# Kernel tuning notes

Hardware: AMD Instinct MI355X
Metric: run time of the kernel (lower is better)

Reference implementation:

```python
import jax, jax.numpy as jnp
import numpy as np

INPUTS, L1, L2, L3 = 40960, 256, 32, 32
B, K = 16384, 32  # batch, fixed active features per side


def setup_inputs() -> dict:
    key = jax.random.key(0)
    ks = jax.random.split(key, 12)
    wf = jax.random.randint(ks[0], (B * K,), 0, INPUTS, dtype=jnp.int64)
    bf = jax.random.randint(ks[1], (B * K,), 0, INPUTS, dtype=jnp.int64)
    offs = jnp.arange(B, dtype=jnp.int64) * K
    stm = jax.random.uniform(ks[2], (B,), dtype=jnp.float32)
    table = jax.random.normal(ks[3], (INPUTS, L1), dtype=jnp.float32) * 0.01
    ft_bias = jnp.zeros((L1,), dtype=jnp.float32)
    # xavier_uniform bounds: sqrt(6/(fan_in+fan_out))
    def xavier(k, shape):
        bound = np.sqrt(6.0 / (shape[0] + shape[1]))
        return jax.random.uniform(k, shape, jnp.float32, -bound, bound)
    W1 = xavier(ks[4], (L2, 2 * L1)); b1 = jnp.zeros((L2,), jnp.float32)
    W2 = xavier(ks[5], (L3, L2));     b2 = jnp.zeros((L3,), jnp.float32)
    Wo = xavier(ks[6], (1, L3));      bo = jnp.zeros((1,), jnp.float32)
    return {"white_features": wf, "white_offsets": offs, "black_features": bf,
            "black_offsets": offs, "stm": stm, "table": table, "ft_bias": ft_bias,
            "W1": W1, "b1": b1, "W2": W2, "b2": b2, "Wo": Wo, "bo": bo}


def _crelu(x):
    return jnp.clip(x, 0.0, 1.0)


def reference(white_features, white_offsets, black_features, black_offsets, stm,
              table, ft_bias, W1, b1, W2, b2, Wo, bo):
    nb = white_offsets.shape[0]
    # Uniform-bag EmbeddingBag(mode='sum'): gather rows and sum within each bag.
    w_acc = table[white_features.reshape(nb, -1)].sum(axis=1) + ft_bias  # [B, L1]
    b_acc = table[black_features.reshape(nb, -1)].sum(axis=1) + ft_bias  # [B, L1]
    wtm = jnp.concatenate([w_acc, b_acc], axis=1)  # [B, 2*L1]
    btm = jnp.concatenate([b_acc, w_acc], axis=1)
    s = stm.reshape(-1, 1)
    x = _crelu(s * wtm + (1.0 - s) * btm)
    x = _crelu(x @ W1.T + b1)
    x = _crelu(x @ W2.T + b2)
    return (x @ Wo.T + bo).squeeze(1)  # [B]
```

## Files before the change

### kernel.cpp

```cpp
#include <hip/hip_runtime.h>

#define KFEAT 32
#define NB 8
#define XPITCH 544
#define APITCH 272

__device__ __forceinline__ float clip01(float v) {
    return fminf(fmaxf(v, 0.0f), 1.0f);
}

__global__ __launch_bounds__(256) void quantize_table_i8(
    const float* __restrict__ src, uint* __restrict__ qt,
    float* __restrict__ scales, int nrows)
{
    const int row = blockIdx.x * 4 + (threadIdx.x >> 6);
    const int l   = threadIdx.x & 63;
    if (row >= nrows) return;

    const float4 v = reinterpret_cast<const float4*>(src)[(size_t)row * 64 + l];
    float m = fmaxf(fmaxf(fabsf(v.x), fabsf(v.y)), fmaxf(fabsf(v.z), fabsf(v.w)));
    m = fmaxf(m, __shfl_xor(m, 1));
    m = fmaxf(m, __shfl_xor(m, 2));
    m = fmaxf(m, __shfl_xor(m, 4));
    m = fmaxf(m, __shfl_xor(m, 8));
    m = fmaxf(m, __shfl_xor(m, 16));
    m = fmaxf(m, __shfl_xor(m, 32));

    const float inv = (m > 0.0f) ? 127.0f / m : 0.0f;
    const int b0 = ((int)rintf(v.x * inv)) & 0xFF;
    const int b1 = ((int)rintf(v.y * inv)) & 0xFF;
    const int b2 = ((int)rintf(v.z * inv)) & 0xFF;
    const int b3 = ((int)rintf(v.w * inv)) & 0xFF;
    qt[(size_t)row * 64 + l] = (uint)b0 | ((uint)b1 << 8) | ((uint)b2 << 16) | ((uint)b3 << 24);
    if (l == 0) scales[row] = m * (1.0f / 127.0f);
}

__global__ __launch_bounds__(256, 8) void nnue_i8_kernel(
    const int* __restrict__ wf, const int* __restrict__ bf,
    const float* __restrict__ stm, const uint* __restrict__ qt,
    const float* __restrict__ scales,
    const float* __restrict__ ft_bias,
    const float* __restrict__ W1, const float* __restrict__ b1,
    const float* __restrict__ W2, const float* __restrict__ b2,
    const float* __restrict__ Wo, const float* __restrict__ bo,
    float* __restrict__ out)
{
    __shared__ float lds[NB * XPITCH];
    __shared__ float y1s[NB][32];

    const int t   = threadIdx.x;
    const int l   = t & 63;
    const int w   = t >> 6;
    const int sub = l & 31;
    const int b0  = blockIdx.x * NB;

    {
        const int side = w & 1;
        const int eb   = w >> 1;
        const int* fp  = side ? bf : wf;

        #pragma unroll
        for (int g = 0; g < 4; ++g) {
            const int bag  = g * 4 + w;
            const int iv   = fp[(size_t)(b0 + 2 * g + eb) * KFEAT + sub];
            float a0 = 0.f, a1 = 0.f, a2 = 0.f, a3 = 0.f;
            #pragma unroll
            for (int k = 0; k < KFEAT; ++k) {
                const int row  = __builtin_amdgcn_readlane(iv, k);
                const int  q   = (int)qt[(size_t)row * 64 + l];
                const float sc = scales[row];
                a0 = fmaf((float)((q << 24) >> 24), sc, a0);
                a1 = fmaf((float)((q << 16) >> 24), sc, a1);
                a2 = fmaf((float)((q <<  8) >> 24), sc, a2);
                a3 = fmaf((float)( q        >> 24), sc, a3);
            }
            *reinterpret_cast<float4*>(&lds[bag * APITCH + l * 4]) =
                make_float4(a0, a1, a2, a3);
        }
    }
    __syncthreads();

    {
        const int e = t >> 5, r = t & 31;
        const float s  = stm[b0 + e];
        const float os = 1.0f - s;
        const float4 wa0 = *reinterpret_cast<const float4*>(&lds[(2 * e + 0) * APITCH + 4 * r]);
        const float4 ba0 = *reinterpret_cast<const float4*>(&lds[(2 * e + 1) * APITCH + 4 * r]);
        const float4 wa1 = *reinterpret_cast<const float4*>(&lds[(2 * e + 0) * APITCH + 4 * (r + 32)]);
        const float4 ba1 = *reinterpret_cast<const float4*>(&lds[(2 * e + 1) * APITCH + 4 * (r + 32)]);
        const float4 fb0 = reinterpret_cast<const float4*>(ft_bias)[r];
        const float4 fb1 = reinterpret_cast<const float4*>(ft_bias)[r + 32];
        __syncthreads();

        #define MIXW(wa, ba, fb, i, hf)                                              \
        {                                                                            \
            float4 xv;                                                               \
            if (hf == 0) {                                                           \
                xv.x = clip01(fmaf(s, (wa).x, fmaf(os, (ba).x, (fb).x)));            \
                xv.y = clip01(fmaf(s, (wa).y, fmaf(os, (ba).y, (fb).y)));            \
                xv.z = clip01(fmaf(s, (wa).z, fmaf(os, (ba).z, (fb).z)));            \
                xv.w = clip01(fmaf(s, (wa).w, fmaf(os, (ba).w, (fb).w)));            \
            } else {                                                                 \
                xv.x = clip01(fmaf(s, (ba).x, fmaf(os, (wa).x, (fb).x)));            \
                xv.y = clip01(fmaf(s, (ba).y, fmaf(os, (wa).y, (fb).y)));            \
                xv.z = clip01(fmaf(s, (ba).z, fmaf(os, (wa).z, (fb).z)));            \
                xv.w = clip01(fmaf(s, (ba).w, fmaf(os, (wa).w, (fb).w)));            \
            }                                                                        \
            const int d = (hf) * 256 + 4 * (i);                                      \
            *reinterpret_cast<float4*>(&lds[e * XPITCH + (d >> 6) * 68 + (d & 63)]) = xv; \
        }
        MIXW(wa0, ba0, fb0, r,      0)
        MIXW(wa1, ba1, fb1, r + 32, 0)
        MIXW(wa0, ba0, fb0, r,      1)
        MIXW(wa1, ba1, fb1, r + 32, 1)
        #undef MIXW
    }
    __syncthreads();

    {
        const int j = t >> 3;
        const int c = t & 7;
        const float* w1p = W1 + j * 512 + c * 64;
        float acc[NB] = {0.f, 0.f, 0.f, 0.f, 0.f, 0.f, 0.f, 0.f};
        #pragma unroll
        for (int blk = 0; blk < 4; ++blk) {
            const float4 wv0 = reinterpret_cast<const float4*>(w1p + blk * 16)[0];
            const float4 wv1 = reinterpret_cast<const float4*>(w1p + blk * 16)[1];
            const float4 wv2 = reinterpret_cast<const float4*>(w1p + blk * 16)[2];
            const float4 wv3 = reinterpret_cast<const float4*>(w1p + blk * 16)[3];
            #pragma unroll
            for (int e = 0; e < NB; ++e) {
                const float* xp = &lds[e * XPITCH + c * 68 + blk * 16];
                const float4 x0 = *reinterpret_cast<const float4*>(xp + 0);
                const float4 x1 = *reinterpret_cast<const float4*>(xp + 4);
                const float4 x2 = *reinterpret_cast<const float4*>(xp + 8);
                const float4 x3 = *reinterpret_cast<const float4*>(xp + 12);
                float a = acc[e];
                a = fmaf(wv0.x, x0.x, a); a = fmaf(wv0.y, x0.y, a);
                a = fmaf(wv0.z, x0.z, a); a = fmaf(wv0.w, x0.w, a);
                a = fmaf(wv1.x, x1.x, a); a = fmaf(wv1.y, x1.y, a);
                a = fmaf(wv1.z, x1.z, a); a = fmaf(wv1.w, x1.w, a);
                a = fmaf(wv2.x, x2.x, a); a = fmaf(wv2.y, x2.y, a);
                a = fmaf(wv2.z, x2.z, a); a = fmaf(wv2.w, x2.w, a);
                a = fmaf(wv3.x, x3.x, a); a = fmaf(wv3.y, x3.y, a);
                a = fmaf(wv3.z, x3.z, a); a = fmaf(wv3.w, x3.w, a);
                acc[e] = a;
            }
        }
        #pragma unroll
        for (int e = 0; e < NB; ++e) {
            acc[e] += __shfl_xor(acc[e], 1);
            acc[e] += __shfl_xor(acc[e], 2);
            acc[e] += __shfl_xor(acc[e], 4);
        }
        if (c == 0) {
            const float bj = b1[j];
            #pragma unroll
            for (int e = 0; e < NB; ++e)
                y1s[e][j] = clip01(acc[e] + bj);
        }
    }
    __syncthreads();

    {
        const int e = t >> 5, i = t & 31;
        const float4* w2p = reinterpret_cast<const float4*>(W2 + i * 32);
        float a2 = b2[i];
        #pragma unroll
        for (int kq = 0; kq < 8; ++kq) {
            const float4 wq = w2p[kq];
            const float4 yq = *reinterpret_cast<const float4*>(&y1s[e][kq * 4]);
            a2 = fmaf(wq.x, yq.x, a2); a2 = fmaf(wq.y, yq.y, a2);
            a2 = fmaf(wq.z, yq.z, a2); a2 = fmaf(wq.w, yq.w, a2);
        }
        a2 = clip01(a2);
        float p = a2 * Wo[i];
        p += __shfl_xor(p, 1);  p += __shfl_xor(p, 2);
        p += __shfl_xor(p, 4);  p += __shfl_xor(p, 8);
        p += __shfl_xor(p, 16);
        if (i == 0) out[b0 + e] = p + bo[0];
    }
}

__global__ __launch_bounds__(256, 6) void nnue_fused_kernel(
    const int* __restrict__ wf, const int* __restrict__ bf,
    const float* __restrict__ stm, const float* __restrict__ table,
    const float* __restrict__ ft_bias,
    const float* __restrict__ W1, const float* __restrict__ b1,
    const float* __restrict__ W2, const float* __restrict__ b2,
    const float* __restrict__ Wo, const float* __restrict__ bo,
    float* __restrict__ out)
{
    __shared__ float4 accs[4][64];
    __shared__ float  xs[2 * 4 * 132];
    __shared__ float  y1s[2][32];

    const int t    = threadIdx.x;
    const int l    = t & 63;
    const int w    = t >> 6;
    const int side = w & 1;
    const int esub = w >> 1;

    const float4 ftb4 = reinterpret_cast<const float4*>(ft_bias)[l];
    const int*   fptr = side ? bf : wf;

    const int j = t >> 3;
    const int c = t & 7;
    const float* w1p = W1 + j * 512 + c * 64;
    const float* x0p = &xs[(0 * 4 + (c >> 1)) * 132 + (c & 1) * 64];
    const float* x1p = &xs[(1 * 4 + (c >> 1)) * 132 + (c & 1) * 64];

    for (int it = 0; it < 8 / 2; ++it) {
        const int b0 = blockIdx.x * 8 + it * 2;

        int idxv = fptr[(size_t)(b0 + esub) * KFEAT + (l & 31)];
        float4 acc = ftb4;
        #pragma unroll
        for (int k = 0; k < KFEAT; ++k) {
            const int row = __builtin_amdgcn_readlane(idxv, k);
            const float4 v = reinterpret_cast<const float4*>(table)[(size_t)row * 64 + l];
            acc.x += v.x; acc.y += v.y; acc.z += v.z; acc.w += v.w;
        }
        accs[w][l] = acc;
        __syncthreads();

        {
            const int e  = t >> 7;
            const int hf = (t >> 6) & 1;
            const int i  = t & 63;
            const float s  = stm[b0 + e];
            const float os = 1.0f - s;
            const float4 wa = accs[e * 2 + 0][i];
            const float4 ba = accs[e * 2 + 1][i];
            float4 x;
            if (hf == 0) {
                x.x = clip01(s * wa.x + os * ba.x);
                x.y = clip01(s * wa.y + os * ba.y);
                x.z = clip01(s * wa.z + os * ba.z);
                x.w = clip01(s * wa.w + os * ba.w);
            } else {
                x.x = clip01(s * ba.x + os * wa.x);
                x.y = clip01(s * ba.y + os * wa.y);
                x.z = clip01(s * ba.z + os * wa.z);
                x.w = clip01(s * ba.w + os * wa.w);
            }
            const int slot = hf * 64 + i;
            const int g = slot >> 5, i4 = slot & 31;
            *reinterpret_cast<float4*>(&xs[(e * 4 + g) * 132 + i4 * 4]) = x;
        }
        __syncthreads();

        float a0 = 0.0f, a1 = 0.0f;
        #pragma unroll 16
        for (int ii = 0; ii < 64; ++ii) {
            const float wv = w1p[ii];
            a0 = fmaf(wv, x0p[ii], a0);
            a1 = fmaf(wv, x1p[ii], a1);
        }
        a0 += __shfl_xor(a0, 1); a0 += __shfl_xor(a0, 2); a0 += __shfl_xor(a0, 4);
        a1 += __shfl_xor(a1, 1); a1 += __shfl_xor(a1, 2); a1 += __shfl_xor(a1, 4);
        if (c == 0) {
            const float bj = b1[j];
            y1s[0][j] = clip01(a0 + bj);
            y1s[1][j] = clip01(a1 + bj);
        }
        __syncthreads();

        if (t < 64) {
            const int e = t >> 5, i = t & 31;
            float a2 = b2[i];
            #pragma unroll
            for (int k2 = 0; k2 < 32; ++k2)
                a2 = fmaf(y1s[e][k2], W2[i * 32 + k2], a2);
            a2 = clip01(a2);
            float p = a2 * Wo[i];
            p += __shfl_xor(p, 1);  p += __shfl_xor(p, 2);
            p += __shfl_xor(p, 4);  p += __shfl_xor(p, 8);
            p += __shfl_xor(p, 16);
            if (i == 0) out[b0 + e] = p + bo[0];
        }
        __syncthreads();
    }
}

extern "C" void kernel_launch(void* const* d_in, const int* in_sizes, int n_in,
                              void* d_out, int out_size, void* d_ws, size_t ws_size,
                              hipStream_t stream) {
    const int*   wf      = (const int*)  d_in[0];
    const int*   bf      = (const int*)  d_in[2];
    const float* stm     = (const float*)d_in[4];
    const float* table   = (const float*)d_in[5];
    const float* ft_bias = (const float*)d_in[6];
    const float* W1      = (const float*)d_in[7];
    const float* b1      = (const float*)d_in[8];
    const float* W2      = (const float*)d_in[9];
    const float* b2      = (const float*)d_in[10];
    const float* Wo      = (const float*)d_in[11];
    const float* bo      = (const float*)d_in[12];
    float*       out     = (float*)d_out;

    const int B = in_sizes[1];
    const int tbl_elems = in_sizes[5];
    const int nrows = tbl_elems / 256;
    const size_t qbytes = (size_t)tbl_elems;
    const size_t need = qbytes + (size_t)nrows * sizeof(float);

    if (ws_size >= need) {
        uint*  qt     = (uint*)d_ws;
        float* scales = (float*)((char*)d_ws + qbytes);
        quantize_table_i8<<<(nrows + 3) / 4, 256, 0, stream>>>(table, qt, scales, nrows);
        nnue_i8_kernel<<<B / NB, 256, 0, stream>>>(
            wf, bf, stm, qt, scales, ft_bias, W1, b1, W2, b2, Wo, bo, out);
    } else {
        nnue_fused_kernel<<<B / 8, 256, 0, stream>>>(
            wf, bf, stm, table, ft_bias, W1, b1, W2, b2, Wo, bo, out);
    }
}
```

Before: 61.54 us.

## Double-buffer embedding row gathers via async global-to-LDS loads

Replaces the per-feature register loads of the int8 table with global_load_lds DMA into a per-wave two-slot LDS staging buffer. Groups of eight rows are issued one step ahead and consumed after an explicit vmcnt wait, so gather latency overlaps dequantize-accumulate work. It also loosens the launch-bounds occupancy hint from 8 to 4 and adds 16 KB of LDS staging per block. This may lower occupancy, and the hand-placed waitcnt and sched_barrier ordering is fragile.

```diff
diff --git a/kernel.cpp b/kernel.cpp
--- a/kernel.cpp
+++ b/kernel.cpp
@@ -35,7 +35,7 @@
     if (l == 0) scales[row] = m * (1.0f / 127.0f);
 }
 
-__global__ __launch_bounds__(256, 8) void nnue_i8_kernel(
+__global__ __launch_bounds__(256, 4) void nnue_i8_async(
     const int* __restrict__ wf, const int* __restrict__ bf,
     const float* __restrict__ stm, const uint* __restrict__ qt,
     const float* __restrict__ scales,
@@ -47,6 +47,7 @@
 {
     __shared__ float lds[NB * XPITCH];
     __shared__ float y1s[NB][32];
+    __shared__ uint  stage[4][2][8 * 64];
 
     const int t   = threadIdx.x;
     const int l   = t & 63;
@@ -59,24 +60,95 @@
         const int eb   = w >> 1;
         const int* fp  = side ? bf : wf;
 
-        #pragma unroll
-        for (int g = 0; g < 4; ++g) {
-            const int bag  = g * 4 + w;
-            const int iv   = fp[(size_t)(b0 + 2 * g + eb) * KFEAT + sub];
-            float a0 = 0.f, a1 = 0.f, a2 = 0.f, a3 = 0.f;
-            #pragma unroll
-            for (int k = 0; k < KFEAT; ++k) {
-                const int row  = __builtin_amdgcn_readlane(iv, k);
-                const int  q   = (int)qt[(size_t)row * 64 + l];
-                const float sc = scales[row];
-                a0 = fmaf((float)((q << 24) >> 24), sc, a0);
-                a1 = fmaf((float)((q << 16) >> 24), sc, a1);
-                a2 = fmaf((float)((q <<  8) >> 24), sc, a2);
-                a3 = fmaf((float)( q        >> 24), sc, a3);
-            }
-            *reinterpret_cast<float4*>(&lds[bag * APITCH + l * 4]) =
+        int ivs[4];
+        #pragma unroll
+        for (int g = 0; g < 4; ++g)
+            ivs[g] = fp[(size_t)(b0 + 2 * g + eb) * KFEAT + sub];
+
+        float a0 = 0.f, a1 = 0.f, a2 = 0.f, a3 = 0.f;
+
+        #define GLD1(iv, kk, sb, j)                                                  \
+        {                                                                            \
+            const int row_ = __builtin_amdgcn_readlane((iv), (kk));                  \
+            __builtin_amdgcn_global_load_lds(                                        \
+                (const __attribute__((address_space(1))) void*)(qt + (size_t)row_ * 64 + l), \
+                (__attribute__((address_space(3))) void*)((sb) + (j) * 64),          \
+                4, 0, 0);                                                            \
+        }
+        #define ISSUE_OCT(o)                                                         \
+        {                                                                            \
+            const int iv_ = ivs[(o) >> 2];                                           \
+            uint* sb_ = &stage[w][(o) & 1][0];                                       \
+            GLD1(iv_, ((o) & 3) * 8 + 0, sb_, 0)                                     \
+            GLD1(iv_, ((o) & 3) * 8 + 1, sb_, 1)                                     \
+            GLD1(iv_, ((o) & 3) * 8 + 2, sb_, 2)                                     \
+            GLD1(iv_, ((o) & 3) * 8 + 3, sb_, 3)                                     \
+            GLD1(iv_, ((o) & 3) * 8 + 4, sb_, 4)                                     \
+            GLD1(iv_, ((o) & 3) * 8 + 5, sb_, 5)                                     \
+            GLD1(iv_, ((o) & 3) * 8 + 6, sb_, 6)                                     \
+            GLD1(iv_, ((o) & 3) * 8 + 7, sb_, 7)                                     \
+        }
+        #define CONS1(iv, kk, sb, j)                                                 \
+        {                                                                            \
+            const int row_  = __builtin_amdgcn_readlane((iv), (kk));                 \
+            const float sc_ = scales[row_];                                          \
+            const int q_    = (int)(sb)[(j) * 64 + l];                               \
+            a0 = fmaf((float)((q_ << 24) >> 24), sc_, a0);                           \
+            a1 = fmaf((float)((q_ << 16) >> 24), sc_, a1);                           \
+            a2 = fmaf((float)((q_ <<  8) >> 24), sc_, a2);                           \
+            a3 = fmaf((float)( q_        >> 24), sc_, a3);                           \
+        }
+        #define CONS_OCT(o)                                                          \
+        {                                                                            \
+            const int iv_ = ivs[(o) >> 2];                                           \
+            const uint* sb_ = &stage[w][(o) & 1][0];                                 \
+            CONS1(iv_, ((o) & 3) * 8 + 0, sb_, 0)                                    \
+            CONS1(iv_, ((o) & 3) * 8 + 1, sb_, 1)                                    \
+            CONS1(iv_, ((o) & 3) * 8 + 2, sb_, 2)                                    \
+            CONS1(iv_, ((o) & 3) * 8 + 3, sb_, 3)                                    \
+            CONS1(iv_, ((o) & 3) * 8 + 4, sb_, 4)                                    \
+            CONS1(iv_, ((o) & 3) * 8 + 5, sb_, 5)                                    \
+            CONS1(iv_, ((o) & 3) * 8 + 6, sb_, 6)                                    \
+            CONS1(iv_, ((o) & 3) * 8 + 7, sb_, 7)                                    \
+        }
+        #define WAITVM8 { asm volatile("s_waitcnt vmcnt(8)" ::: "memory"); __builtin_amdgcn_sched_barrier(0); }
+        #define WAITVM0 { asm volatile("s_waitcnt vmcnt(0)" ::: "memory"); __builtin_amdgcn_sched_barrier(0); }
+        #define FLGKM   { asm volatile("s_waitcnt lgkmcnt(0)" ::: "memory"); __builtin_amdgcn_sched_barrier(0); }
+        #define STORE_BAG(g)                                                         \
+            *reinterpret_cast<float4*>(&lds[((g) * 4 + w) * APITCH + l * 4]) =       \
                 make_float4(a0, a1, a2, a3);
-        }
+
+        ISSUE_OCT(0)
+        ISSUE_OCT(1)
+        WAITVM8  CONS_OCT(0)   FLGKM  ISSUE_OCT(2)
+        WAITVM8  CONS_OCT(1)   FLGKM  ISSUE_OCT(3)
+        WAITVM8  CONS_OCT(2)   FLGKM  ISSUE_OCT(4)
+        WAITVM8  CONS_OCT(3)   FLGKM  ISSUE_OCT(5)
+        STORE_BAG(0)  a0 = a1 = a2 = a3 = 0.f;
+        WAITVM8  CONS_OCT(4)   FLGKM  ISSUE_OCT(6)
+        WAITVM8  CONS_OCT(5)   FLGKM  ISSUE_OCT(7)
+        WAITVM8  CONS_OCT(6)   FLGKM  ISSUE_OCT(8)
+        WAITVM8  CONS_OCT(7)   FLGKM  ISSUE_OCT(9)
+        STORE_BAG(1)  a0 = a1 = a2 = a3 = 0.f;
+        WAITVM8  CONS_OCT(8)   FLGKM  ISSUE_OCT(10)
+        WAITVM8  CONS_OCT(9)   FLGKM  ISSUE_OCT(11)
+        WAITVM8  CONS_OCT(10)  FLGKM  ISSUE_OCT(12)
+        WAITVM8  CONS_OCT(11)  FLGKM  ISSUE_OCT(13)
+        STORE_BAG(2)  a0 = a1 = a2 = a3 = 0.f;
+        WAITVM8  CONS_OCT(12)  FLGKM  ISSUE_OCT(14)
+        WAITVM8  CONS_OCT(13)  FLGKM  ISSUE_OCT(15)
+        WAITVM8  CONS_OCT(14)
+        WAITVM0  CONS_OCT(15)
+        STORE_BAG(3)
+
+        #undef GLD1
+        #undef ISSUE_OCT
+        #undef CONS1
+        #undef CONS_OCT
+        #undef WAITVM8
+        #undef WAITVM0
+        #undef FLGKM
+        #undef STORE_BAG
     }
     __syncthreads();
 
@@ -309,7 +381,7 @@
         uint*  qt     = (uint*)d_ws;
         float* scales = (float*)((char*)d_ws + qbytes);
         quantize_table_i8<<<(nrows + 3) / 4, 256, 0, stream>>>(table, qt, scales, nrows);
-        nnue_i8_kernel<<<B / NB, 256, 0, stream>>>(
+        nnue_i8_async<<<B / NB, 256, 0, stream>>>(
             wf, bf, stm, qt, scales, ft_bias, W1, b1, W2, b2, Wo, bo, out);
     } else {
         nnue_fused_kernel<<<B / 8, 256, 0, stream>>>(
```

Measured after the change: 65.37 us. 6.2% more time.

## Compute first dense layer with fp16 MFMA instead of scalar FMAs

Applied to the files above, without the earlier changes.

Converts W1 to fp16 in a small pre-kernel and stores the activations as swizzled fp16 in LDS. The 8-sample × 512 → 32 layer then runs as 16x16x32 f16 MFMA tiles, with the 8 sample rows zero-padded to 16 and the two K halves reduced through LDS. This replaces a scalar FP32 FMA loop plus shuffle reductions with matrix-core instructions, at the cost of fp16 rounding, an extra launch, and half of each MFMA tile spent on padding.

```diff
diff --git a/kernel.cpp b/kernel.cpp
--- a/kernel.cpp
+++ b/kernel.cpp
@@ -2,8 +2,11 @@
 
 #define KFEAT 32
 #define NB 8
-#define XPITCH 544
 #define APITCH 272
+
+typedef _Float16 f16x8 __attribute__((ext_vector_type(8)));
+typedef _Float16 f16x4 __attribute__((ext_vector_type(4)));
+typedef float    f32x4 __attribute__((ext_vector_type(4)));
 
 __device__ __forceinline__ float clip01(float v) {
     return fminf(fmaxf(v, 0.0f), 1.0f);
@@ -35,18 +38,29 @@
     if (l == 0) scales[row] = m * (1.0f / 127.0f);
 }
 
-__global__ __launch_bounds__(256, 8) void nnue_i8_kernel(
+__global__ __launch_bounds__(256) void convert_w1_f16(
+    const float* __restrict__ W1, _Float16* __restrict__ W1h, int n)
+{
+    const int i = blockIdx.x * 256 + threadIdx.x;
+    if (i < n) W1h[i] = (_Float16)W1[i];
+}
+
+__global__ __launch_bounds__(256, 8) void nnue_i8_mfma(
     const int* __restrict__ wf, const int* __restrict__ bf,
     const float* __restrict__ stm, const uint* __restrict__ qt,
     const float* __restrict__ scales,
+    const _Float16* __restrict__ W1h,
     const float* __restrict__ ft_bias,
-    const float* __restrict__ W1, const float* __restrict__ b1,
+    const float* __restrict__ b1,
     const float* __restrict__ W2, const float* __restrict__ b2,
     const float* __restrict__ Wo, const float* __restrict__ bo,
     float* __restrict__ out)
 {
-    __shared__ float lds[NB * XPITCH];
+    __shared__ float lds[16 * APITCH];
     __shared__ float y1s[NB][32];
+    __shared__ f32x4 cred[2][64];
+
+    char* xhb = reinterpret_cast<char*>(lds);
 
     const int t   = threadIdx.x;
     const int l   = t & 63;
@@ -61,8 +75,8 @@
 
         #pragma unroll
         for (int g = 0; g < 4; ++g) {
-            const int bag  = g * 4 + w;
-            const int iv   = fp[(size_t)(b0 + 2 * g + eb) * KFEAT + sub];
+            const int bag = g * 4 + w;
+            const int iv  = fp[(size_t)(b0 + 2 * g + eb) * KFEAT + sub];
             float a0 = 0.f, a1 = 0.f, a2 = 0.f, a3 = 0.f;
             #pragma unroll
             for (int k = 0; k < KFEAT; ++k) {
@@ -91,6 +105,8 @@
         const float4 fb0 = reinterpret_cast<const float4*>(ft_bias)[r];
         const float4 fb1 = reinterpret_cast<const float4*>(ft_bias)[r + 32];
         __syncthreads();
+
+        const int eswz = e << 3;
 
         #define MIXW(wa, ba, fb, i, hf)                                              \
         {                                                                            \
@@ -106,58 +122,55 @@
                 xv.z = clip01(fmaf(s, (ba).z, fmaf(os, (wa).z, (fb).z)));            \
                 xv.w = clip01(fmaf(s, (ba).w, fmaf(os, (wa).w, (fb).w)));            \
             }                                                                        \
-            const int d = (hf) * 256 + 4 * (i);                                      \
-            *reinterpret_cast<float4*>(&lds[e * XPITCH + (d >> 6) * 68 + (d & 63)]) = xv; \
+            const int k_ = (hf) * 256 + 4 * (i);                                     \
+            f16x4 hv;                                                                \
+            hv[0] = (_Float16)xv.x; hv[1] = (_Float16)xv.y;                          \
+            hv[2] = (_Float16)xv.z; hv[3] = (_Float16)xv.w;                          \
+            *reinterpret_cast<f16x4*>(xhb + e * 1024 + ((k_ ^ eswz) << 1)) = hv;     \
         }
         MIXW(wa0, ba0, fb0, r,      0)
         MIXW(wa1, ba1, fb1, r + 32, 0)
         MIXW(wa0, ba0, fb0, r,      1)
         MIXW(wa1, ba1, fb1, r + 32, 1)
         #undef MIXW
+
+        *reinterpret_cast<uint4*>(xhb + 8192 + t * 32)      = make_uint4(0, 0, 0, 0);
+        *reinterpret_cast<uint4*>(xhb + 8192 + t * 32 + 16) = make_uint4(0, 0, 0, 0);
     }
     __syncthreads();
 
     {
-        const int j = t >> 3;
-        const int c = t & 7;
-        const float* w1p = W1 + j * 512 + c * 64;
-        float acc[NB] = {0.f, 0.f, 0.f, 0.f, 0.f, 0.f, 0.f, 0.f};
+        const int ntile = w & 1;
+        const int khalf = w >> 1;
+        const int col   = l & 15;
+        const int krow  = l >> 4;
+        const int neuron = ntile * 16 + col;
+        const int rswz   = (col & 7) << 3;
+
+        f32x4 acc = {0.f, 0.f, 0.f, 0.f};
+        const _Float16* bp = W1h + neuron * 512 + khalf * 256 + krow * 8;
+
         #pragma unroll
-        for (int blk = 0; blk < 4; ++blk) {
-            const float4 wv0 = reinterpret_cast<const float4*>(w1p + blk * 16)[0];
-            const float4 wv1 = reinterpret_cast<const float4*>(w1p + blk * 16)[1];
-            const float4 wv2 = reinterpret_cast<const float4*>(w1p + blk * 16)[2];
-            const float4 wv3 = reinterpret_cast<const float4*>(w1p + blk * 16)[3];
-            #pragma unroll
-            for (int e = 0; e < NB; ++e) {
-                const float* xp = &lds[e * XPITCH + c * 68 + blk * 16];
-                const float4 x0 = *reinterpret_cast<const float4*>(xp + 0);
-                const float4 x1 = *reinterpret_cast<const float4*>(xp + 4);
-                const float4 x2 = *reinterpret_cast<const float4*>(xp + 8);
-                const float4 x3 = *reinterpret_cast<const float4*>(xp + 12);
-                float a = acc[e];
-                a = fmaf(wv0.x, x0.x, a); a = fmaf(wv0.y, x0.y, a);
-                a = fmaf(wv0.z, x0.z, a); a = fmaf(wv0.w, x0.w, a);
-                a = fmaf(wv1.x, x1.x, a); a = fmaf(wv1.y, x1.y, a);
-                a = fmaf(wv1.z, x1.z, a); a = fmaf(wv1.w, x1.w, a);
-                a = fmaf(wv2.x, x2.x, a); a = fmaf(wv2.y, x2.y, a);
-                a = fmaf(wv2.z, x2.z, a); a = fmaf(wv2.w, x2.w, a);
-                a = fmaf(wv3.x, x3.x, a); a = fmaf(wv3.y, x3.y, a);
-                a = fmaf(wv3.z, x3.z, a); a = fmaf(wv3.w, x3.w, a);
-                acc[e] = a;
+        for (int s = 0; s < 8; ++s) {
+            const int k = khalf * 256 + s * 32 + krow * 8;
+            const f16x8 a = *reinterpret_cast<const f16x8*>(
+                xhb + col * 1024 + ((k ^ rswz) << 1));
+            const f16x8 b = *reinterpret_cast<const f16x8*>(bp + s * 32);
+            acc = __builtin_amdgcn_mfma_f32_16x16x32_f16(a, b, acc, 0, 0, 0);
+        }
+
+        if (khalf == 1) cred[ntile][l] = acc;
+        __syncthreads();
+        if (khalf == 0) {
+            const f32x4 o = cred[ntile][l];
+            const float bn = b1[neuron];
+            if (krow < 2) {
+                #pragma unroll
+                for (int reg = 0; reg < 4; ++reg) {
+                    const int r8 = krow * 4 + reg;
+                    y1s[r8][neuron] = clip01(acc[reg] + o[reg] + bn);
+                }
             }
-        }
-        #pragma unroll
-        for (int e = 0; e < NB; ++e) {
-            acc[e] += __shfl_xor(acc[e], 1);
-            acc[e] += __shfl_xor(acc[e], 2);
-            acc[e] += __shfl_xor(acc[e], 4);
-        }
-        if (c == 0) {
-            const float bj = b1[j];
-            #pragma unroll
-            for (int e = 0; e < NB; ++e)
-                y1s[e][j] = clip01(acc[e] + bj);
         }
     }
     __syncthreads();
@@ -302,15 +315,20 @@
     const int B = in_sizes[1];
     const int tbl_elems = in_sizes[5];
     const int nrows = tbl_elems / 256;
+    const int w1_elems = in_sizes[7];
     const size_t qbytes = (size_t)tbl_elems;
-    const size_t need = qbytes + (size_t)nrows * sizeof(float);
+    const size_t sbytes = (size_t)nrows * sizeof(float);
+    const size_t hbytes = (size_t)w1_elems * sizeof(_Float16);
+    const size_t need = qbytes + sbytes + hbytes;
 
     if (ws_size >= need) {
-        uint*  qt     = (uint*)d_ws;
-        float* scales = (float*)((char*)d_ws + qbytes);
+        uint*      qt     = (uint*)d_ws;
+        float*     scales = (float*)((char*)d_ws + qbytes);
+        _Float16*  W1h    = (_Float16*)((char*)d_ws + qbytes + sbytes);
         quantize_table_i8<<<(nrows + 3) / 4, 256, 0, stream>>>(table, qt, scales, nrows);
-        nnue_i8_kernel<<<B / NB, 256, 0, stream>>>(
-            wf, bf, stm, qt, scales, ft_bias, W1, b1, W2, b2, Wo, bo, out);
+        convert_w1_f16<<<(w1_elems + 255) / 256, 256, 0, stream>>>(W1, W1h, w1_elems);
+        nnue_i8_mfma<<<B / NB, 256, 0, stream>>>(
+            wf, bf, stm, qt, scales, W1h, ft_bias, b1, W2, b2, Wo, bo, out);
     } else {
         nnue_fused_kernel<<<B / 8, 256, 0, stream>>>(
             wf, bf, stm, table, ft_bias, W1, b1, W2, b2, Wo, bo, out);
```

New measurement: 55.51 us. -9.8%, faster.
